# Optimization experiments

Hardware: AMD Instinct MI355X
Metric: run time of the kernel (lower is better)

The kernel has to match this reference:

```python
import jax, jax.numpy as jnp
import numpy as np

N_NODES = 100000
N_EDGES = 800000
IN_FEAT = 128


def setup_inputs() -> dict:
    key = jax.random.key(0)
    k_feat, k_src, k_dst, k_w1, k_b1, k_w2 = jax.random.split(key, 6)
    feature = jax.random.normal(k_feat, (N_NODES, IN_FEAT), dtype=jnp.float32)
    src = jax.random.randint(k_src, (N_EDGES,), 0, N_NODES, dtype=jnp.int64)
    dst = jax.random.randint(k_dst, (N_EDGES,), 0, N_NODES, dtype=jnp.int64)
    # nn.Linear params: y = x @ W.T + b; Kaiming-uniform-ish init scale
    lim1 = 1.0 / np.sqrt(2 * IN_FEAT)
    W1 = jax.random.uniform(k_w1, (IN_FEAT, 2 * IN_FEAT), jnp.float32, -lim1, lim1)
    b1 = jax.random.uniform(k_b1, (IN_FEAT,), jnp.float32, -lim1, lim1)
    lim2 = 1.0 / np.sqrt(IN_FEAT)
    W2 = jax.random.uniform(k_w2, (1, IN_FEAT), jnp.float32, -lim2, lim2)
    b2 = jnp.zeros((1,), jnp.float32)
    return {"feature": feature, "src": src, "dst": dst,
            "W1": W1, "b1": b1, "W2": W2, "b2": b2}


def reference(feature, src, dst, W1, b1, W2, b2):
    # gather src/dst node feats and concat -> [E, 2*in_feat]
    h = jnp.concatenate([feature[src], feature[dst]], axis=1)
    # 2-layer MLP per edge: Linear -> ReLU -> Linear
    hid = jax.nn.relu(h @ W1.T + b1)            # [E, in_feat]
    score = hid @ W2.T + b2                      # [E, 1]
    return score
```

## Files before the change

### kernel.cpp

```cpp
#include <hip/hip_runtime.h>
#include <stdint.h>

typedef short short8 __attribute__((ext_vector_type(8)));
typedef float floatx4 __attribute__((ext_vector_type(4)));

#define NN 100000
#define NE 800000
#define KF 128
#define PC 256
#define BM 64
#define LDK 136

__device__ __forceinline__ unsigned short f2bf(float x) {
  union { float f; unsigned u; } c; c.f = x;
  unsigned u = c.u + 0x7FFFu + ((c.u >> 16) & 1u);
  return (unsigned short)(u >> 16);
}
__device__ __forceinline__ float bfl(unsigned u) {
  union { unsigned u; float f; } c; c.u = u << 16; return c.f;
}
__device__ __forceinline__ float bfh(unsigned u) {
  union { unsigned u; float f; } c; c.u = u & 0xFFFF0000u; return c.f;
}

extern "C" __global__ void __launch_bounds__(256)
node_proj_kernel(const float* __restrict__ feature,
                 const float* __restrict__ W1,
                 const float* __restrict__ b1,
                 unsigned short* __restrict__ P)
{
  __shared__ unsigned short Wl[128 * LDK];
  __shared__ unsigned short Al[BM * LDK];
  __shared__ float b1l[128];

  const int t = threadIdx.x;
  const int nodeBase = blockIdx.x * BM;

  #pragma unroll
  for (int it = 0; it < 4; ++it) {
    int c  = t + it * 256;
    int nl = c >> 4;
    int kc = (c & 15) << 3;
    int node = nodeBase + nl;
    float4 f0 = make_float4(0.f, 0.f, 0.f, 0.f);
    float4 f1 = make_float4(0.f, 0.f, 0.f, 0.f);
    if (node < NN) {
      const float* fp = feature + (size_t)node * KF + kc;
      f0 = ((const float4*)fp)[0];
      f1 = ((const float4*)fp)[1];
    }
    short8 v;
    v[0] = (short)f2bf(f0.x); v[1] = (short)f2bf(f0.y);
    v[2] = (short)f2bf(f0.z); v[3] = (short)f2bf(f0.w);
    v[4] = (short)f2bf(f1.x); v[5] = (short)f2bf(f1.y);
    v[6] = (short)f2bf(f1.z); v[7] = (short)f2bf(f1.w);
    *(short8*)&Al[nl * LDK + kc] = v;
  }
  if (t < 128) b1l[t] = b1[t];

  const int wave = t >> 6;
  const int lane = t & 63;
  const int m16  = lane & 15;
  const int quad = lane >> 4;

  short8 a0, a1, a2, a3;
  bool aLoaded = false;

  for (int half = 0; half < 2; ++half) {
    #pragma unroll
    for (int it = 0; it < 8; ++it) {
      int c  = t + it * 256;
      int jl = c >> 4;
      int kc = (c & 15) << 3;
      const float* sp = W1 + jl * 256 + half * 128 + kc;
      float4 f0 = ((const float4*)sp)[0];
      float4 f1 = ((const float4*)sp)[1];
      short8 v;
      v[0] = (short)f2bf(f0.x); v[1] = (short)f2bf(f0.y);
      v[2] = (short)f2bf(f0.z); v[3] = (short)f2bf(f0.w);
      v[4] = (short)f2bf(f1.x); v[5] = (short)f2bf(f1.y);
      v[6] = (short)f2bf(f1.z); v[7] = (short)f2bf(f1.w);
      *(short8*)&Wl[jl * LDK + kc] = v;
    }
    __syncthreads();

    if (!aLoaded) {
      const unsigned short* arow = &Al[(wave * 16 + m16) * LDK + quad * 8];
      a0 = *(const short8*)(arow + 0);
      a1 = *(const short8*)(arow + 32);
      a2 = *(const short8*)(arow + 64);
      a3 = *(const short8*)(arow + 96);
      aLoaded = true;
    }

    #pragma unroll
    for (int nt = 0; nt < 8; ++nt) {
      floatx4 acc = {0.f, 0.f, 0.f, 0.f};
      const unsigned short* wrow = &Wl[(nt * 16 + m16) * LDK + quad * 8];
      acc = __builtin_amdgcn_mfma_f32_16x16x32_bf16(a0, *(const short8*)(wrow +  0), acc, 0, 0, 0);
      acc = __builtin_amdgcn_mfma_f32_16x16x32_bf16(a1, *(const short8*)(wrow + 32), acc, 0, 0, 0);
      acc = __builtin_amdgcn_mfma_f32_16x16x32_bf16(a2, *(const short8*)(wrow + 64), acc, 0, 0, 0);
      acc = __builtin_amdgcn_mfma_f32_16x16x32_bf16(a3, *(const short8*)(wrow + 96), acc, 0, 0, 0);

      int n = half * 128 + nt * 16 + m16;
      float bias = (half == 0) ? b1l[nt * 16 + m16] : 0.f;
      #pragma unroll
      for (int r = 0; r < 4; ++r) {
        int node = nodeBase + wave * 16 + quad * 4 + r;
        if (node < NN) P[(size_t)node * PC + n] = f2bf(acc[r] + bias);
      }
    }
    __syncthreads();
  }
}

__device__ __forceinline__ float dot8(const uint4 u1, const uint4 u2,
                                      const float4 wA, const float4 wB)
{
  float acc = 0.f, x;
  x = fmaxf(bfl(u1.x) + bfl(u2.x), 0.f); acc += x * wA.x;
  x = fmaxf(bfh(u1.x) + bfh(u2.x), 0.f); acc += x * wA.y;
  x = fmaxf(bfl(u1.y) + bfl(u2.y), 0.f); acc += x * wA.z;
  x = fmaxf(bfh(u1.y) + bfh(u2.y), 0.f); acc += x * wA.w;
  x = fmaxf(bfl(u1.z) + bfl(u2.z), 0.f); acc += x * wB.x;
  x = fmaxf(bfh(u1.z) + bfh(u2.z), 0.f); acc += x * wB.y;
  x = fmaxf(bfl(u1.w) + bfl(u2.w), 0.f); acc += x * wB.z;
  x = fmaxf(bfh(u1.w) + bfh(u2.w), 0.f); acc += x * wB.w;
  return acc;
}

extern "C" __global__ void __launch_bounds__(256)
edge_score_kernel(const unsigned short* __restrict__ P,
                  const int* __restrict__ src,
                  const int* __restrict__ dst,
                  const float* __restrict__ W2,
                  const float* __restrict__ b2,
                  float* __restrict__ out)
{
  const int t    = threadIdx.x;
  const int lane = t & 15;
  const int g    = t >> 4;
  const int e0   = blockIdx.x * 64 + g * 4;
  if (e0 >= NE) return;

  const int4 sv = *(const int4*)(src + e0);
  const int4 dv = *(const int4*)(dst + e0);

  const unsigned short* Ps = P + lane * 8;
  const unsigned short* Pd = P + 128 + lane * 8;

  const uint4 A0 = *(const uint4*)(Ps + (size_t)sv.x * PC);
  const uint4 B0 = *(const uint4*)(Pd + (size_t)dv.x * PC);
  const uint4 A1 = *(const uint4*)(Ps + (size_t)sv.y * PC);
  const uint4 B1 = *(const uint4*)(Pd + (size_t)dv.y * PC);
  const uint4 A2 = *(const uint4*)(Ps + (size_t)sv.z * PC);
  const uint4 B2 = *(const uint4*)(Pd + (size_t)dv.z * PC);
  const uint4 A3 = *(const uint4*)(Ps + (size_t)sv.w * PC);
  const uint4 B3 = *(const uint4*)(Pd + (size_t)dv.w * PC);

  const float4 wA = *(const float4*)(W2 + lane * 8);
  const float4 wB = *(const float4*)(W2 + lane * 8 + 4);

  float r0 = dot8(A0, B0, wA, wB);
  float r1 = dot8(A1, B1, wA, wB);
  float r2 = dot8(A2, B2, wA, wB);
  float r3 = dot8(A3, B3, wA, wB);

  r0 += __shfl_xor(r0, 8); r1 += __shfl_xor(r1, 8);
  r2 += __shfl_xor(r2, 8); r3 += __shfl_xor(r3, 8);
  r0 += __shfl_xor(r0, 4); r1 += __shfl_xor(r1, 4);
  r2 += __shfl_xor(r2, 4); r3 += __shfl_xor(r3, 4);
  r0 += __shfl_xor(r0, 2); r1 += __shfl_xor(r1, 2);
  r2 += __shfl_xor(r2, 2); r3 += __shfl_xor(r3, 2);
  r0 += __shfl_xor(r0, 1); r1 += __shfl_xor(r1, 1);
  r2 += __shfl_xor(r2, 1); r3 += __shfl_xor(r3, 1);

  if (lane == 0) {
    const float bb = b2[0];
    float4 o;
    o.x = r0 + bb; o.y = r1 + bb; o.z = r2 + bb; o.w = r3 + bb;
    *(float4*)(out + e0) = o;
  }
}

extern "C" void kernel_launch(void* const* d_in, const int* in_sizes, int n_in,
                              void* d_out, int out_size, void* d_ws, size_t ws_size,
                              hipStream_t stream)
{
  const float* feature = (const float*)d_in[0];
  const int*   src     = (const int*)d_in[1];
  const int*   dst     = (const int*)d_in[2];
  const float* W1      = (const float*)d_in[3];
  const float* b1      = (const float*)d_in[4];
  const float* W2      = (const float*)d_in[5];
  const float* b2      = (const float*)d_in[6];
  float* out = (float*)d_out;
  unsigned short* P = (unsigned short*)d_ws;

  dim3 grid1((NN + BM - 1) / BM);
  node_proj_kernel<<<grid1, 256, 0, stream>>>(feature, W1, b1, P);

  dim3 grid2((NE + 63) / 64);
  edge_score_kernel<<<grid2, 256, 0, stream>>>(P, src, dst, W2, b2, out);
}
```

Before: 171.5 us.

## Pre-convert W1 to swizzled bf16 once and stream it into LDS directly

```diff
diff --git a/kernel.cpp b/kernel.cpp
--- a/kernel.cpp
+++ b/kernel.cpp
@@ -24,17 +24,50 @@
 }
 
 extern "C" __global__ void __launch_bounds__(256)
+wcat_prep_kernel(const float* __restrict__ W1, unsigned short* __restrict__ Wcatb)
+{
+  const int idx = blockIdx.x * 256 + threadIdx.x;
+  const int j  = idx >> 4;
+  const int k8 = (idx & 15) << 3;
+
+  const int h  = j >> 7;
+  const int jl = j & 127;
+  const float* sp = W1 + (size_t)jl * 256 + h * 128 + k8;
+  const float4 f0 = ((const float4*)sp)[0];
+  const float4 f1 = ((const float4*)sp)[1];
+
+  short8 v;
+  v[0] = (short)f2bf(f0.x); v[1] = (short)f2bf(f0.y);
+  v[2] = (short)f2bf(f0.z); v[3] = (short)f2bf(f0.w);
+  v[4] = (short)f2bf(f1.x); v[5] = (short)f2bf(f1.y);
+  v[6] = (short)f2bf(f1.z); v[7] = (short)f2bf(f1.w);
+
+  const unsigned lin = (unsigned)jl * 256u + (unsigned)k8 * 2u;
+  const unsigned swz = lin ^ ((unsigned)(jl & 7) << 4);
+  *(short8*)((char*)Wcatb + h * 32768 + swz) = v;
+}
+
+extern "C" __global__ void __launch_bounds__(256)
 node_proj_kernel(const float* __restrict__ feature,
-                 const float* __restrict__ W1,
+                 const unsigned short* __restrict__ Wcatb,
                  const float* __restrict__ b1,
                  unsigned short* __restrict__ P)
 {
-  __shared__ unsigned short Wl[128 * LDK];
+  __shared__ unsigned short Wl[128 * 128];
   __shared__ unsigned short Al[BM * LDK];
   __shared__ float b1l[128];
 
   const int t = threadIdx.x;
   const int nodeBase = blockIdx.x * BM;
+
+  #pragma unroll
+  for (int it = 0; it < 8; ++it) {
+    int c = t + it * 256;
+    __builtin_amdgcn_global_load_lds(
+        (const __attribute__((address_space(1))) void*)((const char*)Wcatb + c * 16),
+        (__attribute__((address_space(3))) void*)((char*)Wl + c * 16),
+        16, 0, 0);
+  }
 
   #pragma unroll
   for (int it = 0; it < 4; ++it) {
@@ -67,21 +100,6 @@
   bool aLoaded = false;
 
   for (int half = 0; half < 2; ++half) {
-    #pragma unroll
-    for (int it = 0; it < 8; ++it) {
-      int c  = t + it * 256;
-      int jl = c >> 4;
-      int kc = (c & 15) << 3;
-      const float* sp = W1 + jl * 256 + half * 128 + kc;
-      float4 f0 = ((const float4*)sp)[0];
-      float4 f1 = ((const float4*)sp)[1];
-      short8 v;
-      v[0] = (short)f2bf(f0.x); v[1] = (short)f2bf(f0.y);
-      v[2] = (short)f2bf(f0.z); v[3] = (short)f2bf(f0.w);
-      v[4] = (short)f2bf(f1.x); v[5] = (short)f2bf(f1.y);
-      v[6] = (short)f2bf(f1.z); v[7] = (short)f2bf(f1.w);
-      *(short8*)&Wl[jl * LDK + kc] = v;
-    }
     __syncthreads();
 
     if (!aLoaded) {
@@ -96,21 +114,35 @@
     #pragma unroll
     for (int nt = 0; nt < 8; ++nt) {
       floatx4 acc = {0.f, 0.f, 0.f, 0.f};
-      const unsigned short* wrow = &Wl[(nt * 16 + m16) * LDK + quad * 8];
-      acc = __builtin_amdgcn_mfma_f32_16x16x32_bf16(a0, *(const short8*)(wrow +  0), acc, 0, 0, 0);
-      acc = __builtin_amdgcn_mfma_f32_16x16x32_bf16(a1, *(const short8*)(wrow + 32), acc, 0, 0, 0);
-      acc = __builtin_amdgcn_mfma_f32_16x16x32_bf16(a2, *(const short8*)(wrow + 64), acc, 0, 0, 0);
-      acc = __builtin_amdgcn_mfma_f32_16x16x32_bf16(a3, *(const short8*)(wrow + 96), acc, 0, 0, 0);
-
-      int n = half * 128 + nt * 16 + m16;
-      float bias = (half == 0) ? b1l[nt * 16 + m16] : 0.f;
+      const int j = nt * 16 + m16;
+      const unsigned base = (unsigned)j * 256u + (unsigned)quad * 16u;
+      const unsigned msk  = (unsigned)(j & 7) << 4;
+      const char* WlB = (const char*)Wl;
+      acc = __builtin_amdgcn_mfma_f32_16x16x32_bf16(a0, *(const short8*)(WlB + ((base +   0u) ^ msk)), acc, 0, 0, 0);
+      acc = __builtin_amdgcn_mfma_f32_16x16x32_bf16(a1, *(const short8*)(WlB + ((base +  64u) ^ msk)), acc, 0, 0, 0);
+      acc = __builtin_amdgcn_mfma_f32_16x16x32_bf16(a2, *(const short8*)(WlB + ((base + 128u) ^ msk)), acc, 0, 0, 0);
+      acc = __builtin_amdgcn_mfma_f32_16x16x32_bf16(a3, *(const short8*)(WlB + ((base + 192u) ^ msk)), acc, 0, 0, 0);
+
+      const int n = half * 128 + j;
+      const float bias = (half == 0) ? b1l[j] : 0.f;
       #pragma unroll
       for (int r = 0; r < 4; ++r) {
         int node = nodeBase + wave * 16 + quad * 4 + r;
         if (node < NN) P[(size_t)node * PC + n] = f2bf(acc[r] + bias);
       }
     }
-    __syncthreads();
+
+    if (half == 0) {
+      __syncthreads();
+      #pragma unroll
+      for (int it = 0; it < 8; ++it) {
+        int c = t + it * 256;
+        __builtin_amdgcn_global_load_lds(
+            (const __attribute__((address_space(1))) void*)((const char*)Wcatb + 32768 + c * 16),
+            (__attribute__((address_space(3))) void*)((char*)Wl + c * 16),
+            16, 0, 0);
+      }
+    }
   }
 }
 
@@ -196,9 +228,13 @@
   const float* b2      = (const float*)d_in[6];
   float* out = (float*)d_out;
   unsigned short* P = (unsigned short*)d_ws;
+  unsigned short* Wcatb = (unsigned short*)d_out;
+
+  dim3 gridW(16);
+  wcat_prep_kernel<<<gridW, 256, 0, stream>>>(W1, Wcatb);
 
   dim3 grid1((NN + BM - 1) / BM);
-  node_proj_kernel<<<grid1, 256, 0, stream>>>(feature, W1, b1, P);
+  node_proj_kernel<<<grid1, 256, 0, stream>>>(feature, Wcatb, b1, P);
 
   dim3 grid2((NE + 63) / 64);
   edge_score_kernel<<<grid2, 256, 0, stream>>>(P, src, dst, W2, b2, out);
```

After: 170.4 us. Within noise of the previous version (-0.7%).
